# Kernel optimization log

Measured on AMD Instinct MI355X. Metric: run time of the kernel, lower is better.

Reference implementation:

```python
import jax, jax.numpy as jnp
import numpy as np

OUT, IN = 4096, 4096
BLOCK = 32
NBLK = IN // BLOCK  # 128


def setup_inputs() -> dict:
    key = jax.random.key(0)
    k1, k2, k3 = jax.random.split(key, 3)
    x = jax.random.normal(k1, (2, 2048, IN), dtype=jnp.float32)
    # per-block scales (GGUF stores fp16 scales; small magnitude typical)
    scales = jax.random.normal(k2, (OUT, NBLK), dtype=jnp.float32) * 0.01
    # int8 codes stored as unsigned 0..255; signed value = code - 128
    codes = jax.random.randint(k3, (OUT, NBLK, BLOCK), 0, 256, dtype=jnp.int32)
    return {"x": x, "scales": scales, "codes": codes}


def dequantize_q8_0(scales, codes):
    # scales: [out, nblk], codes: [out, nblk, 32] unsigned -> signed int8 semantics
    signed = codes.astype(jnp.float32) - 128.0
    w = scales[:, :, None] * signed            # [out, nblk, 32]
    return w.reshape(OUT, IN)                   # [out, in]


def reference(x, scales, codes):
    weight = dequantize_q8_0(scales, codes)     # [out, in]
    # nn.functional.linear: y = x @ weight.T
    return jnp.einsum("bsi,oi->bso", x, weight)
```

## Files before the change

kernel.cpp:

```cpp
#include <hip/hip_runtime.h>
#include <stdint.h>


#define M_DIM 4096
#define N_DIM 4096
#define K_DIM 4096

typedef __attribute__((ext_vector_type(8))) short bf16x8;
typedef __attribute__((ext_vector_type(4))) float f32x4;

__device__ __forceinline__ unsigned short f32_to_bf16_rne(float f) {
    unsigned u = __float_as_uint(f);
    u += 0x7fffu + ((u >> 16) & 1u);
    return (unsigned short)(u >> 16);
}

__device__ __forceinline__ void load_lds16(const void* g, void* l) {
    __builtin_amdgcn_global_load_lds(
        (const __attribute__((address_space(1))) unsigned int*)g,
        (__attribute__((address_space(3))) unsigned int*)l, 16, 0, 0);
}

__global__ __launch_bounds__(256) void prologue_kernel(
        const int* __restrict__ codes, const float* __restrict__ scales,
        unsigned short* __restrict__ W,
        const float* __restrict__ x, unsigned short* __restrict__ xb) {
    const int bid = blockIdx.x;
    if (bid < 16384) {
        const int tid = bid * 256 + threadIdx.x;
        const float s = scales[tid >> 3];
        const int4 c  = ((const int4*)codes)[tid];
        union { unsigned short u[4]; uint2 v; } p;
        p.u[0] = f32_to_bf16_rne(s * (float)(c.x - 128));
        p.u[1] = f32_to_bf16_rne(s * (float)(c.y - 128));
        p.u[2] = f32_to_bf16_rne(s * (float)(c.z - 128));
        p.u[3] = f32_to_bf16_rne(s * (float)(c.w - 128));
        ((uint2*)W)[tid] = p.v;
    } else {
        const int tid = (bid - 16384) * 256 + threadIdx.x;
        const float4 f = ((const float4*)x)[tid];
        union { unsigned short u[4]; uint2 v; } p;
        p.u[0] = f32_to_bf16_rne(f.x); p.u[1] = f32_to_bf16_rne(f.y);
        p.u[2] = f32_to_bf16_rne(f.z); p.u[3] = f32_to_bf16_rne(f.w);
        ((uint2*)xb)[tid] = p.v;
    }
}

#define BAR()   asm volatile("s_barrier" ::: "memory")
#define VMC(N)  asm volatile("s_waitcnt vmcnt(" #N ")" ::: "memory")
#define SB0()   __builtin_amdgcn_sched_barrier(0)

__global__ __launch_bounds__(512, 2) void gemm_8phase(
        const unsigned short* __restrict__ A,
        const unsigned short* __restrict__ B,
        float* __restrict__ C) {
    __shared__ unsigned short sA[2][2][256 * 32];
    __shared__ unsigned short sB[2][2][256 * 32];

    const int tid  = threadIdx.x;
    const int wave = tid >> 6;
    const int lane = tid & 63;

    const int bid  = blockIdx.x;
    const int xcd  = bid & 7;
    const int slot = bid >> 3;
    const int m0 = ((xcd >> 2) * 8 + (slot >> 2)) * 256;
    const int n0 = ((xcd & 3) * 4 + (slot & 3)) * 256;

    const int srow   = lane >> 2;
    const int schunk = (lane & 3) ^ ((lane >> 3) & 3);
    const unsigned short* Ag = A + (size_t)(m0 + wave * 32 + srow) * K_DIM + schunk * 8;
    const unsigned short* Bg = B + (size_t)(n0 + wave * 32 + srow) * K_DIM + schunk * 8;
    const int ldsW = wave * 1024;

    const int frow = lane & 15;
    const int quad = lane >> 4;
    const int wm = wave >> 2;
    const int wn = wave & 3;
    const int cswz = (quad ^ ((frow >> 1) & 3)) * 8;
    const int aOff = (wm * 128 + frow) * 32 + cswz;
    const int bOff = (wn * 64 + frow) * 32 + cswz;

    f32x4 acc[8][4] = {};
    bf16x8 aX[4], aY[4], b0r[4], b1r[4];

#define STG_A(BUF, KH, KT) do { \
        const unsigned short* s_ = Ag + (size_t)(KT) * 64 + (KH) * 32; \
        load_lds16(s_,                       &sA[BUF][KH][ldsW]); \
        load_lds16(s_ + (size_t)16 * K_DIM,  &sA[BUF][KH][ldsW + 512]); \
    } while (0)
#define STG_B(BUF, KH, KT) do { \
        const unsigned short* s_ = Bg + (size_t)(KT) * 64 + (KH) * 32; \
        load_lds16(s_,                       &sB[BUF][KH][ldsW]); \
        load_lds16(s_ + (size_t)16 * K_DIM,  &sB[BUF][KH][ldsW + 512]); \
    } while (0)
#define RD_A4(DST, BUF, KH, MH) do { _Pragma("unroll") \
        for (int i_ = 0; i_ < 4; ++i_) \
            DST[i_] = *(const bf16x8*)&sA[BUF][KH][aOff + ((MH) * 4 + i_) * 512]; \
    } while (0)
#define RD_B4(DST, BUF, KH) do { _Pragma("unroll") \
        for (int i_ = 0; i_ < 4; ++i_) \
            DST[i_] = *(const bf16x8*)&sB[BUF][KH][bOff + i_ * 512]; \
    } while (0)
#define MM16(AR, BR, MH) do { _Pragma("unroll") \
        for (int i_ = 0; i_ < 4; ++i_) { _Pragma("unroll") \
            for (int n_ = 0; n_ < 4; ++n_) \
                acc[(MH) * 4 + i_][n_] = __builtin_amdgcn_mfma_f32_16x16x32_bf16( \
                    AR[i_], BR[n_], acc[(MH) * 4 + i_][n_], 0, 0, 0); \
        } } while (0)

#define KTILE(BUF, OBUF, T, I0, I1, I2, I3, VM2, VM3, R3) do { \
         \
        RD_A4(aY, BUF, 0, 1); \
        if (I0) { STG_A(OBUF, 1, (T) + 1); } \
        BAR(); SB0(); \
        __builtin_amdgcn_s_setprio(1); MM16(aX, b0r, 0); __builtin_amdgcn_s_setprio(0); \
        BAR(); \
         \
        RD_A4(aX, BUF, 1, 0); RD_B4(b1r, BUF, 1); \
        if (I1) { STG_B(BUF, 0, (T) + 2); } \
        BAR(); SB0(); \
        __builtin_amdgcn_s_setprio(1); MM16(aY, b0r, 1); __builtin_amdgcn_s_setprio(0); \
        BAR(); \
         \
        RD_A4(aY, BUF, 1, 1); \
        if (I2) { STG_A(BUF, 0, (T) + 2); } \
        BAR(); SB0(); \
        __builtin_amdgcn_s_setprio(1); MM16(aX, b1r, 0); __builtin_amdgcn_s_setprio(0); \
        VM2; BAR(); \
         \
        if (R3) { RD_A4(aX, OBUF, 0, 0); RD_B4(b0r, OBUF, 0); } \
        if (I3) { STG_B(BUF, 1, (T) + 2); } \
        BAR(); SB0(); \
        __builtin_amdgcn_s_setprio(1); MM16(aY, b1r, 1); __builtin_amdgcn_s_setprio(0); \
        VM3; BAR(); \
    } while (0)

    STG_A(0, 0, 0); STG_B(0, 0, 0); STG_A(0, 1, 0); STG_B(0, 1, 0);
    STG_B(1, 0, 1); STG_A(1, 0, 1); STG_B(1, 1, 1);
    VMC(6); BAR();
    RD_A4(aX, 0, 0, 0); RD_B4(b0r, 0, 0);

#pragma unroll 1
    for (int t2 = 0; t2 < 31; ++t2) {
        const int t = t2 * 2;
        KTILE(0, 1, t,     1, 1, 1, 1, VMC(8), VMC(6), 1);
        KTILE(1, 0, t + 1, 1, 1, 1, 1, VMC(8), VMC(6), 1);
    }
    KTILE(0, 1, 62, 1, 0, 0, 0, VMC(4), VMC(0), 1);
    KTILE(1, 0, 63, 0, 0, 0, 0, (void)0, (void)0, 0);

    const size_t crow0 = (size_t)(m0 + wm * 128 + quad * 4);
    const int    ccol  = n0 + wn * 64 + frow;
#pragma unroll
    for (int mt = 0; mt < 8; ++mt)
#pragma unroll
        for (int nt = 0; nt < 4; ++nt)
#pragma unroll
            for (int r = 0; r < 4; ++r)
                C[(crow0 + mt * 16 + r) * N_DIM + ccol + nt * 16] = acc[mt][nt][r];

#undef STG_A
#undef STG_B
#undef RD_A4
#undef RD_B4
#undef MM16
#undef KTILE
}

extern "C" void kernel_launch(void* const* d_in, const int* in_sizes, int n_in,
                              void* d_out, int out_size, void* d_ws, size_t ws_size,
                              hipStream_t stream) {
    const float* x      = (const float*)d_in[0];
    const float* scales = (const float*)d_in[1];
    const int*   codes  = (const int*)d_in[2];
    float* y = (float*)d_out;

    unsigned short* Wb = (unsigned short*)d_ws;
    unsigned short* xb = (unsigned short*)((char*)d_ws + (size_t)N_DIM * K_DIM * 2);

    prologue_kernel<<<32768, 256, 0, stream>>>(codes, scales, Wb, x, xb);

    gemm_8phase<<<256, 512, 0, stream>>>(xb, Wb, y);
}
```

Measured before the change: 288.0 us.

## Replace cross-phase LDS register prefetch with in-phase reads and explicit lgkmcnt waits

Restructures the 8-phase GEMM so each phase reads its own A/B fragments from LDS and waits on lgkmcnt(0) before the MFMAs. Previously each phase prefetched the next phase's fragments and relied on sched_barrier ordering. The change also drops the memory clobbers on the waitcnt asm, uses the builtin barrier, and merges the two vmcnt waits per tile into one at tile end. This simplifies synchronisation, but LDS read latency is no longer hidden behind the preceding MFMA block, and the compiler may reorder around the unclobbered waits.

After: 287.9 us. No clear change (-0.0%).

```diff
diff --git a/kernel.cpp b/kernel.cpp
--- a/kernel.cpp
+++ b/kernel.cpp
@@ -46,9 +46,9 @@
     }
 }
 
-#define BAR()   asm volatile("s_barrier" ::: "memory")
-#define VMC(N)  asm volatile("s_waitcnt vmcnt(" #N ")" ::: "memory")
-#define SB0()   __builtin_amdgcn_sched_barrier(0)
+#define BAR()   __builtin_amdgcn_s_barrier()
+#define LGKM0() asm volatile("s_waitcnt lgkmcnt(0)")
+#define VMC(N)  asm volatile("s_waitcnt vmcnt(" #N ")")
 
 __global__ __launch_bounds__(512, 2) void gemm_8phase(
         const unsigned short* __restrict__ A,
@@ -109,46 +109,45 @@
                     AR[i_], BR[n_], acc[(MH) * 4 + i_][n_], 0, 0, 0); \
         } } while (0)
 
-#define KTILE(BUF, OBUF, T, I0, I1, I2, I3, VM2, VM3, R3) do { \
+#define KTILE(BUF, OBUF, T, I0, I1, I2, I3, VMF) do { \
          \
-        RD_A4(aY, BUF, 0, 1); \
+        RD_A4(aX, BUF, 0, 0); RD_B4(b0r, BUF, 0); \
         if (I0) { STG_A(OBUF, 1, (T) + 1); } \
-        BAR(); SB0(); \
+        BAR(); LGKM0(); \
         __builtin_amdgcn_s_setprio(1); MM16(aX, b0r, 0); __builtin_amdgcn_s_setprio(0); \
         BAR(); \
          \
-        RD_A4(aX, BUF, 1, 0); RD_B4(b1r, BUF, 1); \
+        RD_A4(aY, BUF, 0, 1); \
         if (I1) { STG_B(BUF, 0, (T) + 2); } \
-        BAR(); SB0(); \
+        BAR(); LGKM0(); \
         __builtin_amdgcn_s_setprio(1); MM16(aY, b0r, 1); __builtin_amdgcn_s_setprio(0); \
         BAR(); \
          \
+        RD_A4(aX, BUF, 1, 0); RD_B4(b1r, BUF, 1); \
+        if (I2) { STG_A(BUF, 0, (T) + 2); } \
+        BAR(); LGKM0(); \
+        __builtin_amdgcn_s_setprio(1); MM16(aX, b1r, 0); __builtin_amdgcn_s_setprio(0); \
+        BAR(); \
+         \
         RD_A4(aY, BUF, 1, 1); \
-        if (I2) { STG_A(BUF, 0, (T) + 2); } \
-        BAR(); SB0(); \
-        __builtin_amdgcn_s_setprio(1); MM16(aX, b1r, 0); __builtin_amdgcn_s_setprio(0); \
-        VM2; BAR(); \
-         \
-        if (R3) { RD_A4(aX, OBUF, 0, 0); RD_B4(b0r, OBUF, 0); } \
         if (I3) { STG_B(BUF, 1, (T) + 2); } \
-        BAR(); SB0(); \
+        BAR(); LGKM0(); \
         __builtin_amdgcn_s_setprio(1); MM16(aY, b1r, 1); __builtin_amdgcn_s_setprio(0); \
-        VM3; BAR(); \
+        VMF; BAR(); \
     } while (0)
 
     STG_A(0, 0, 0); STG_B(0, 0, 0); STG_A(0, 1, 0); STG_B(0, 1, 0);
     STG_B(1, 0, 1); STG_A(1, 0, 1); STG_B(1, 1, 1);
     VMC(6); BAR();
-    RD_A4(aX, 0, 0, 0); RD_B4(b0r, 0, 0);
 
 #pragma unroll 1
     for (int t2 = 0; t2 < 31; ++t2) {
         const int t = t2 * 2;
-        KTILE(0, 1, t,     1, 1, 1, 1, VMC(8), VMC(6), 1);
-        KTILE(1, 0, t + 1, 1, 1, 1, 1, VMC(8), VMC(6), 1);
+        KTILE(0, 1, t,     1, 1, 1, 1, VMC(6));
+        KTILE(1, 0, t + 1, 1, 1, 1, 1, VMC(6));
     }
-    KTILE(0, 1, 62, 1, 0, 0, 0, VMC(4), VMC(0), 1);
-    KTILE(1, 0, 63, 0, 0, 0, 0, (void)0, (void)0, 0);
+    KTILE(0, 1, 62, 1, 0, 0, 0, VMC(0));
+    KTILE(1, 0, 63, 0, 0, 0, 0, (void)0);
 
     const size_t crow0 = (size_t)(m0 + wm * 128 + quad * 4);
     const int    ccol  = n0 + wn * 64 + frow;
```
